# Kernel optimization log

Hardware: AMD Instinct MI355X
Metric: run time of the kernel (lower is better)

The kernel has to match this reference:

```python
import jax, jax.numpy as jnp
import numpy as np

B, N, D, H = 4, 2048, 512, 8
KD = D // H  # per-head key/value dim = 64
NORM = 1.0 / np.sqrt(KD).astype(np.float32)


def setup_inputs() -> dict:
    key = jax.random.key(0)
    kq, km, k1, k2, k3 = jax.random.split(key, 5)
    s = 1.0 / np.sqrt(D)
    return {
        "queries": jax.random.normal(kq, (B, N, D), dtype=jnp.float32),
        "mask": jax.random.randint(km, (B, N, N), 0, 2).astype(jnp.bool_),
        "Wq": jax.random.normal(k1, (D, D), dtype=jnp.float32) * s,
        "Wk": jax.random.normal(k2, (D, D), dtype=jnp.float32) * s,
        "Wc": jax.random.normal(k3, (D, D), dtype=jnp.float32) * s,
    }


def reference(queries, mask, Wq, Wk, Wc):
    # Self-attention path (keys=None, values=None): V uses key_embed (Wk).
    Q = (queries @ Wq.T).reshape(B, N, H, KD)  # [B,N,H,kd]
    K = (queries @ Wk.T).reshape(B, N, H, KD)
    V = K  # original code: V = key_embed(queries) when values is None
    scores = NORM * jnp.einsum("bqhd,bkhd->bhqk", Q, K)  # [B,H,N,N]
    scores = jnp.where(mask[:, None, :, :], -jnp.inf, scores)
    attn = jax.nn.softmax(scores, axis=-1)
    out = jnp.einsum("bhqk,bkhd->bqhd", attn, V).reshape(B, N, H * KD)
    return out @ Wc.T  # [B,N,D]
```

## Files before the change

kernel.cpp:

```cpp
#include <hip/hip_runtime.h>
#include <hip/hip_bf16.h>
#include <math.h>

#define B_ 4
#define N_ 2048
#define D_ 512
#define H_ 8
#define NORM2_ 0.18033688011112042f

typedef __attribute__((ext_vector_type(8))) short short8;
typedef __attribute__((ext_vector_type(4))) float f32x4;
#define MFMA16(a, b, c) __builtin_amdgcn_mfma_f32_16x16x32_bf16(a, b, c, 0, 0, 0)
#define EXP2(x) __builtin_amdgcn_exp2f(x)

static __device__ __forceinline__ ushort f2bf(float x) {
  union { float f; uint32_t u; } v; v.f = x;
  const uint32_t r = v.u + 0x7fffu + ((v.u >> 16) & 1u);
  return (ushort)(r >> 16);
}

static __device__ __forceinline__ uint32_t pk2(float lo, float hi) {
  __hip_bfloat162 h = __float22bfloat162_rn(make_float2(lo, hi));
  return *(reinterpret_cast<uint32_t*>(&h));
}

static __device__ __forceinline__ void async16(const ushort* lds, const ushort* g) {
  __builtin_amdgcn_global_load_lds(
      (const __attribute__((address_space(1))) uint32_t*)g,
      (__attribute__((address_space(3))) uint32_t*)(ushort*)lds, 16, 0, 0);
}

__global__ __launch_bounds__(256) void prep(const float* __restrict__ q,
                                            const int* __restrict__ mask,
                                            const float* __restrict__ wq,
                                            const float* __restrict__ wk,
                                            const float* __restrict__ wc,
                                            ushort* __restrict__ Xb,
                                            ushort* __restrict__ Wb,
                                            uint32_t* __restrict__ pk) {
  const int bx = blockIdx.x;
  if (bx < 2048) {
    const int lane = threadIdx.x & 63;
    const int wid = ((bx << 8) + threadIdx.x) >> 6;
    for (int i = wid; i < 65536; i += 8192) {
      const int4 m = ((const int4*)mask)[(size_t)i * 64 + lane];
      uint32_t nib = (uint32_t)(m.x != 0) | ((uint32_t)(m.y != 0) << 1) |
                     ((uint32_t)(m.z != 0) << 2) | ((uint32_t)(m.w != 0) << 3);
      nib |= __shfl_xor(nib, 1) << 4;
      nib |= __shfl_xor(nib, 2) << 8;
      nib |= __shfl_xor(nib, 4) << 16;
      if ((lane & 7) == 0) pk[i * 8 + (lane >> 3)] = nib;
    }
  } else if (bx < 3072) {
    const int i = ((bx - 2048) << 8) + threadIdx.x;
    for (int j = i; j < 1048576; j += 262144) {
      const float4 v = ((const float4*)q)[j];
      uint2 o; o.x = pk2(v.x, v.y); o.y = pk2(v.z, v.w);
      ((uint2*)Xb)[j] = o;
    }
  } else {
    const int i = ((bx - 3072) << 8) + threadIdx.x;
    for (int j = i; j < 196608; j += 24576) {
      const int wi = j >> 16, off = j & 65535;
      const float* src = (wi == 0) ? wq : (wi == 1) ? wk : wc;
      const float4 v = ((const float4*)src)[off];
      uint2 o; o.x = pk2(v.x, v.y); o.y = pk2(v.z, v.w);
      ((uint2*)Wb)[j] = o;
    }
  }
}

template <int F32OUT>
__global__ __launch_bounds__(256) void gemm128(const ushort* __restrict__ X,
                                               const ushort* __restrict__ W0,
                                               const ushort* __restrict__ W1,
                                               void* __restrict__ C0,
                                               void* __restrict__ C1,
                                               float s0, float s1) {
  const ushort* Wp = (blockIdx.z == 0) ? W0 : W1;
  void* Cp = (blockIdx.z == 0) ? C0 : C1;
  const float sc = (blockIdx.z == 0) ? s0 : s1;
  const int t = threadIdx.x;
  const int w = t >> 6, lane = t & 63, quad = lane >> 4, c = lane & 15;
  const int wm = w & 1, wn = w >> 1;
  const int n0 = blockIdx.x * 128, m0 = blockIdx.y * 128;
  __shared__ __align__(16) ushort Xs[128][64];
  __shared__ __align__(16) ushort Ws[128][64];
  f32x4 acc[4][4];
#pragma unroll
  for (int i = 0; i < 4; ++i)
#pragma unroll
    for (int j = 0; j < 4; ++j) acc[i][j] = (f32x4){0.f, 0.f, 0.f, 0.f};

  for (int k0 = 0; k0 < D_; k0 += 64) {
    __syncthreads();
#pragma unroll
    for (int g = 0; g < 4; ++g) {
      const int id = w * 256 + g * 64 + lane;
      const int row = id >> 3, lch = id & 7;
      const int gch = lch ^ (row & 7);
      async16(&Xs[row][lch * 8], X + (size_t)(m0 + row) * D_ + k0 + gch * 8);
      async16(&Ws[row][lch * 8], Wp + (size_t)(n0 + row) * D_ + k0 + gch * 8);
    }
    __syncthreads();
#pragma unroll
    for (int s = 0; s < 2; ++s) {
      short8 af[4], bt[4];
#pragma unroll
      for (int i = 0; i < 4; ++i) {
        const int rA = wn * 64 + i * 16 + c;
        af[i] = *(const short8*)&Ws[rA][(((s * 4 + quad) ^ (rA & 7)) & 7) * 8];
        const int rB = wm * 64 + i * 16 + c;
        bt[i] = *(const short8*)&Xs[rB][(((s * 4 + quad) ^ (rB & 7)) & 7) * 8];
      }
#pragma unroll
      for (int i = 0; i < 4; ++i)
#pragma unroll
        for (int j = 0; j < 4; ++j) acc[i][j] = MFMA16(af[i], bt[j], acc[i][j]);
    }
  }
#pragma unroll
  for (int i = 0; i < 4; ++i)
#pragma unroll
    for (int j = 0; j < 4; ++j) {
      const size_t off =
          (size_t)(m0 + wm * 64 + j * 16 + c) * D_ + n0 + wn * 64 + i * 16 + quad * 4;
      if (F32OUT) {
        float4 v; v.x = acc[i][j][0]; v.y = acc[i][j][1]; v.z = acc[i][j][2]; v.w = acc[i][j][3];
        *(float4*)((float*)Cp + off) = v;
      } else {
        uint2 uv;
        uv.x = pk2(acc[i][j][0] * sc, acc[i][j][1] * sc);
        uv.y = pk2(acc[i][j][2] * sc, acc[i][j][3] * sc);
        *(uint2*)((ushort*)Cp + off) = uv;
      }
    }
}

__global__ __launch_bounds__(256) void attn_mfma(const ushort* __restrict__ Qb,
                                                 const ushort* __restrict__ Kb,
                                                 const uint32_t* __restrict__ pk,
                                                 ushort* __restrict__ Ab) {
  const int qt = blockIdx.x, h = blockIdx.y, b = blockIdx.z;
  const int q0 = qt * 64;
  const int t = threadIdx.x;
  const int w = t >> 6, lane = t & 63, quad = lane >> 4, c = lane & 15;

  __shared__ __align__(16) ushort Ks[2][64][64];
  __shared__ __align__(16) uint32_t KtU[2][64][32];
  __shared__ __align__(16) ushort QP[4][16][72];
  ushort(*Qs)[64] = (ushort(*)[64]) & QP[0][0][0];
  ushort(*Pq)[16][72] = QP;

#pragma unroll
  for (int p = 0; p < 2; ++p) {
    const int id = t + p * 256;
    const int row = id >> 3, lch = id & 7, gch = lch ^ (row & 7);
    async16(&Qs[row][lch * 8], Qb + (size_t)(b * N_ + q0 + row) * D_ + h * 64 + gch * 8);
  }
  __syncthreads();
  const int rq = (w << 4) + c;
  const short8 bq0 = *(const short8*)&Qs[rq][((quad ^ (rq & 7)) & 7) * 8];
  const short8 bq1 = *(const short8*)&Qs[rq][(((4 + quad) ^ (rq & 7)) & 7) * 8];

  short8 vones;
#pragma unroll
  for (int i = 0; i < 8; ++i) vones[i] = (short)0x3F80;

  f32x4 o[4];
#pragma unroll
  for (int i = 0; i < 4; ++i) o[i] = (f32x4){0.f, 0.f, 0.f, 0.f};
  f32x4 o5 = (f32x4){0.f, 0.f, 0.f, 0.f};

  const int kp = t >> 3, ch = t & 7;
  const int r0 = 2 * kp, r1 = r0 + 1;
  const int ksw0 = ((ch ^ (r0 & 7)) & 7) * 8, ksw1 = ((ch ^ (r1 & 7)) & 7) * 8;
  const ushort* kb0 = Kb + (size_t)(b * N_ + 2 * kp) * D_ + h * 64 + ch * 8;
  const uint32_t* pkq = pk + ((size_t)(b * N_ + q0 + (w << 4) + c) << 6);

  {
    const uint4 c0 = *(const uint4*)kb0;
    const uint4 c1 = *(const uint4*)(kb0 + D_);
    *(uint4*)&Ks[0][r0][ksw0] = c0;
    *(uint4*)&Ks[0][r1][ksw1] = c1;
    const uint32_t* a0 = (const uint32_t*)&c0;
    const uint32_t* a1 = (const uint32_t*)&c1;
#pragma unroll
    for (int m = 0; m < 4; ++m) {
      const uint32_t lo = __builtin_amdgcn_perm(a1[m], a0[m], 0x05040100);
      const uint32_t hi = __builtin_amdgcn_perm(a1[m], a0[m], 0x07060302);
      const int j0 = 2 * m, j1 = 2 * m + 1;
      KtU[0][ch * 8 + j0][(kp & 3) | ((((kp >> 2) ^ j0 ^ ch) & 7) << 2)] = lo;
      KtU[0][ch * 8 + j1][(kp & 3) | ((((kp >> 2) ^ j1 ^ ch) & 7) << 2)] = hi;
    }
  }
  uint2 cm = *(const uint2*)pkq;

  const int NT = N_ / 64;
  for (int kt = 0; kt < NT; ++kt) {
    __syncthreads();
    const int cur = kt & 1, nxt = cur ^ 1;

    uint4 nx0, nx1; uint2 nxm;
    const bool more = (kt + 1 < NT);
    if (more) {
      const ushort* kbn = kb0 + (size_t)(kt + 1) * 64 * D_;
      nx0 = *(const uint4*)kbn;
      nx1 = *(const uint4*)(kbn + D_);
      nxm = *(const uint2*)(pkq + (kt + 1) * 2);
    }

#pragma unroll
    for (int tI = 0; tI < 4; ++tI) {
      const int rk = tI * 16 + c;
      const short8 aK0 = *(const short8*)&Ks[cur][rk][((quad ^ (rk & 7)) & 7) * 8];
      const short8 aK1 = *(const short8*)&Ks[cur][rk][(((4 + quad) ^ (rk & 7)) & 7) * 8];
      f32x4 z = (f32x4){0.f, 0.f, 0.f, 0.f};
      z = MFMA16(aK0, bq0, z);
      z = MFMA16(aK1, bq1, z);
      const uint32_t mw = (tI < 2) ? cm.x : cm.y;
      const int bb = ((tI & 1) << 4) + quad * 4;
      uint32_t pb[4];
#pragma unroll
      for (int r = 0; r < 4; ++r) {
        const float sv = ((mw >> (bb + r)) & 1u) ? -INFINITY : z[r];
        pb[r] = __float_as_uint(EXP2(sv));
      }
      const uint32_t pw0 = __builtin_amdgcn_perm(pb[1], pb[0], 0x07060302);
      const uint32_t pw1 = __builtin_amdgcn_perm(pb[3], pb[2], 0x07060302);
      *(uint2*)&Pq[w][c][tI * 16 + quad * 4] = make_uint2(pw0, pw1);
    }

    const short8 bp0 = *(const short8*)&Pq[w][c][quad * 8];
    const short8 bp1 = *(const short8*)&Pq[w][c][32 + quad * 8];
    o5 = MFMA16(vones, bp0, o5);
    o5 = MFMA16(vones, bp1, o5);
#pragma unroll
    for (int dt = 0; dt < 4; ++dt) {
      const int dd = dt * 16 + c;
      const int g = (c & 7) ^ ((2 * dt + (c >> 3)) & 7);
      const short8 aV0 = *(const short8*)&KtU[cur][dd][((quad ^ g) & 7) << 2];
      const short8 aV1 = *(const short8*)&KtU[cur][dd][(((4 + quad) ^ g) & 7) << 2];
      o[dt] = MFMA16(aV0, bp0, o[dt]);
      o[dt] = MFMA16(aV1, bp1, o[dt]);
    }

    if (more) {
      *(uint4*)&Ks[nxt][r0][ksw0] = nx0;
      *(uint4*)&Ks[nxt][r1][ksw1] = nx1;
      const uint32_t* a0 = (const uint32_t*)&nx0;
      const uint32_t* a1 = (const uint32_t*)&nx1;
#pragma unroll
      for (int m = 0; m < 4; ++m) {
        const uint32_t lo = __builtin_amdgcn_perm(a1[m], a0[m], 0x05040100);
        const uint32_t hi = __builtin_amdgcn_perm(a1[m], a0[m], 0x07060302);
        const int j0 = 2 * m, j1 = 2 * m + 1;
        KtU[nxt][ch * 8 + j0][(kp & 3) | ((((kp >> 2) ^ j0 ^ ch) & 7) << 2)] = lo;
        KtU[nxt][ch * 8 + j1][(kp & 3) | ((((kp >> 2) ^ j1 ^ ch) & 7) << 2)] = hi;
      }
      cm = nxm;
    }
  }

  const float inv = 1.f / o5[0];
#pragma unroll
  for (int dt = 0; dt < 4; ++dt) {
    uint2 uv;
    uv.x = pk2(o[dt][0] * inv, o[dt][1] * inv);
    uv.y = pk2(o[dt][2] * inv, o[dt][3] * inv);
    *(uint2*)(Ab + (size_t)(b * N_ + q0 + (w << 4) + c) * D_ + h * 64 + dt * 16 + quad * 4) = uv;
  }
}

extern "C" void kernel_launch(void* const* d_in, const int* in_sizes, int n_in,
                              void* d_out, int out_size, void* d_ws, size_t ws_size,
                              hipStream_t stream) {
  const float* queries = (const float*)d_in[0];
  const int* mask = (const int*)d_in[1];
  const float* Wq = (const float*)d_in[2];
  const float* Wk = (const float*)d_in[3];
  const float* Wc = (const float*)d_in[4];
  float* out = (float*)d_out;

  const size_t nTok = (size_t)B_ * N_;
  const size_t nXD = nTok * D_;
  const size_t nW = (size_t)D_ * D_;
  ushort* Xb = (ushort*)d_ws;
  ushort* Wqb = Xb + nXD;
  ushort* Wkb = Wqb + nW;
  ushort* Wcb = Wkb + nW;
  ushort* Qb = Wcb + nW;
  ushort* Kb = Qb + nXD;
  ushort* Ab = Kb + nXD;
  uint32_t* pk = (uint32_t*)(Ab + nXD);

  prep<<<3168, 256, 0, stream>>>(queries, mask, Wq, Wk, Wc, Xb, Wqb, pk);
  gemm128<0><<<dim3(D_ / 128, (int)(nTok / 128), 2), 256, 0, stream>>>(
      Xb, Wqb, Wkb, Qb, Kb, NORM2_, 1.0f);
  attn_mfma<<<dim3(N_ / 64, H_, B_), 256, 0, stream>>>(Qb, Kb, pk, Ab);
  gemm128<1><<<dim3(D_ / 128, (int)(nTok / 128), 1), 256, 0, stream>>>(
      Ab, Wcb, nullptr, out, nullptr, 1.0f, 1.0f);
}
```

Before: 218.9 us.

## Single-buffer K tiles in LDS with register prefetch and two barriers per step

Replaces the double-buffered K and transposed-K LDS tiles with single buffers. Each iteration now writes the prefetched registers to LDS, syncs, issues the next global load, computes, then rotates registers. This halves the K staging LDS footprint, which may allow more resident blocks, at the cost of an extra barrier per iteration and less overlap between LDS writes and compute. It also applies the mask after exp2 by zeroing the result instead of feeding -inf into exp2, and removes an unused helper.

```diff
diff --git a/kernel.cpp b/kernel.cpp
--- a/kernel.cpp
+++ b/kernel.cpp
@@ -12,12 +12,6 @@
 typedef __attribute__((ext_vector_type(4))) float f32x4;
 #define MFMA16(a, b, c) __builtin_amdgcn_mfma_f32_16x16x32_bf16(a, b, c, 0, 0, 0)
 #define EXP2(x) __builtin_amdgcn_exp2f(x)
-
-static __device__ __forceinline__ ushort f2bf(float x) {
-  union { float f; uint32_t u; } v; v.f = x;
-  const uint32_t r = v.u + 0x7fffu + ((v.u >> 16) & 1u);
-  return (ushort)(r >> 16);
-}
 
 static __device__ __forceinline__ uint32_t pk2(float lo, float hi) {
   __hip_bfloat162 h = __float22bfloat162_rn(make_float2(lo, hi));
@@ -146,8 +140,8 @@
   const int t = threadIdx.x;
   const int w = t >> 6, lane = t & 63, quad = lane >> 4, c = lane & 15;
 
-  __shared__ __align__(16) ushort Ks[2][64][64];
-  __shared__ __align__(16) uint32_t KtU[2][64][32];
+  __shared__ __align__(16) ushort Ks[64][64];
+  __shared__ __align__(16) uint32_t KtU[64][32];
   __shared__ __align__(16) ushort QP[4][16][72];
   ushort(*Qs)[64] = (ushort(*)[64]) & QP[0][0][0];
   ushort(*Pq)[16][72] = QP;
@@ -178,11 +172,16 @@
   const ushort* kb0 = Kb + (size_t)(b * N_ + 2 * kp) * D_ + h * 64 + ch * 8;
   const uint32_t* pkq = pk + ((size_t)(b * N_ + q0 + (w << 4) + c) << 6);
 
-  {
-    const uint4 c0 = *(const uint4*)kb0;
-    const uint4 c1 = *(const uint4*)(kb0 + D_);
-    *(uint4*)&Ks[0][r0][ksw0] = c0;
-    *(uint4*)&Ks[0][r1][ksw1] = c1;
+  uint4 c0 = *(const uint4*)kb0;
+  uint4 c1 = *(const uint4*)(kb0 + D_);
+  uint2 cm = *(const uint2*)pkq;
+  uint4 nx0, nx1; uint2 nxm;
+
+  const int NT = N_ / 64;
+  for (int kt = 0; kt < NT; ++kt) {
+    __syncthreads();
+    *(uint4*)&Ks[r0][ksw0] = c0;
+    *(uint4*)&Ks[r1][ksw1] = c1;
     const uint32_t* a0 = (const uint32_t*)&c0;
     const uint32_t* a1 = (const uint32_t*)&c1;
 #pragma unroll
@@ -190,20 +189,12 @@
       const uint32_t lo = __builtin_amdgcn_perm(a1[m], a0[m], 0x05040100);
       const uint32_t hi = __builtin_amdgcn_perm(a1[m], a0[m], 0x07060302);
       const int j0 = 2 * m, j1 = 2 * m + 1;
-      KtU[0][ch * 8 + j0][(kp & 3) | ((((kp >> 2) ^ j0 ^ ch) & 7) << 2)] = lo;
-      KtU[0][ch * 8 + j1][(kp & 3) | ((((kp >> 2) ^ j1 ^ ch) & 7) << 2)] = hi;
-    }
-  }
-  uint2 cm = *(const uint2*)pkq;
-
-  const int NT = N_ / 64;
-  for (int kt = 0; kt < NT; ++kt) {
-    __syncthreads();
-    const int cur = kt & 1, nxt = cur ^ 1;
-
-    uint4 nx0, nx1; uint2 nxm;
-    const bool more = (kt + 1 < NT);
-    if (more) {
+      KtU[ch * 8 + j0][(kp & 3) | ((((kp >> 2) ^ j0 ^ ch) & 7) << 2)] = lo;
+      KtU[ch * 8 + j1][(kp & 3) | ((((kp >> 2) ^ j1 ^ ch) & 7) << 2)] = hi;
+    }
+    __syncthreads();
+
+    if (kt + 1 < NT) {
       const ushort* kbn = kb0 + (size_t)(kt + 1) * 64 * D_;
       nx0 = *(const uint4*)kbn;
       nx1 = *(const uint4*)(kbn + D_);
@@ -213,8 +204,8 @@
 #pragma unroll
     for (int tI = 0; tI < 4; ++tI) {
       const int rk = tI * 16 + c;
-      const short8 aK0 = *(const short8*)&Ks[cur][rk][((quad ^ (rk & 7)) & 7) * 8];
-      const short8 aK1 = *(const short8*)&Ks[cur][rk][(((4 + quad) ^ (rk & 7)) & 7) * 8];
+      const short8 aK0 = *(const short8*)&Ks[rk][((quad ^ (rk & 7)) & 7) * 8];
+      const short8 aK1 = *(const short8*)&Ks[rk][(((4 + quad) ^ (rk & 7)) & 7) * 8];
       f32x4 z = (f32x4){0.f, 0.f, 0.f, 0.f};
       z = MFMA16(aK0, bq0, z);
       z = MFMA16(aK1, bq1, z);
@@ -223,8 +214,8 @@
       uint32_t pb[4];
 #pragma unroll
       for (int r = 0; r < 4; ++r) {
-        const float sv = ((mw >> (bb + r)) & 1u) ? -INFINITY : z[r];
-        pb[r] = __float_as_uint(EXP2(sv));
+        const float e = EXP2(z[r]);
+        pb[r] = ((mw >> (bb + r)) & 1u) ? 0u : __float_as_uint(e);
       }
       const uint32_t pw0 = __builtin_amdgcn_perm(pb[1], pb[0], 0x07060302);
       const uint32_t pw1 = __builtin_amdgcn_perm(pb[3], pb[2], 0x07060302);
@@ -239,27 +230,13 @@
     for (int dt = 0; dt < 4; ++dt) {
       const int dd = dt * 16 + c;
       const int g = (c & 7) ^ ((2 * dt + (c >> 3)) & 7);
-      const short8 aV0 = *(const short8*)&KtU[cur][dd][((quad ^ g) & 7) << 2];
-      const short8 aV1 = *(const short8*)&KtU[cur][dd][(((4 + quad) ^ g) & 7) << 2];
+      const short8 aV0 = *(const short8*)&KtU[dd][((quad ^ g) & 7) << 2];
+      const short8 aV1 = *(const short8*)&KtU[dd][(((4 + quad) ^ g) & 7) << 2];
       o[dt] = MFMA16(aV0, bp0, o[dt]);
       o[dt] = MFMA16(aV1, bp1, o[dt]);
     }
 
-    if (more) {
-      *(uint4*)&Ks[nxt][r0][ksw0] = nx0;
-      *(uint4*)&Ks[nxt][r1][ksw1] = nx1;
-      const uint32_t* a0 = (const uint32_t*)&nx0;
-      const uint32_t* a1 = (const uint32_t*)&nx1;
-#pragma unroll
-      for (int m = 0; m < 4; ++m) {
-        const uint32_t lo = __builtin_amdgcn_perm(a1[m], a0[m], 0x05040100);
-        const uint32_t hi = __builtin_amdgcn_perm(a1[m], a0[m], 0x07060302);
-        const int j0 = 2 * m, j1 = 2 * m + 1;
-        KtU[nxt][ch * 8 + j0][(kp & 3) | ((((kp >> 2) ^ j0 ^ ch) & 7) << 2)] = lo;
-        KtU[nxt][ch * 8 + j1][(kp & 3) | ((((kp >> 2) ^ j1 ^ ch) & 7) << 2)] = hi;
-      }
-      cm = nxm;
-    }
+    if (kt + 1 < NT) { c0 = nx0; c1 = nx1; cm = nxm; }
   }
 
   const float inv = 1.f / o5[0];
```

After: 211.5 us. 3.4% less time.
